# Performance work log

Measured on AMD Instinct MI355X. Metric: run time of the kernel, lower is better.

The kernel has to match this reference:

```python
import jax, jax.numpy as jnp
import numpy as np

LP = 512   # paragraph length (sequential steps)
LQ = 512   # question/context length attended over
B = 24     # batch_size global in source
IN = 150   # in_size (encoder output dim)
H = 150    # self.hidden_size = 2*75


def setup_inputs() -> dict:
    key = jax.random.key(0)
    ks = jax.random.split(key, 12)
    sc = 1.0 / np.sqrt(2 * IN)  # keep pre-activations in a sane range
    return {
        "up": jax.random.normal(ks[0], (LP, B, IN), jnp.float32),
        "uq": jax.random.normal(ks[1], (LQ, B, IN), jnp.float32),
        "v0": jax.random.normal(ks[2], (B, H), jnp.float32),
        "V": jax.random.normal(ks[3], (B, H, 1), jnp.float32),
        "Wp": jax.random.normal(ks[4], (H, 2 * IN), jnp.float32) * sc,
        "Wq": jax.random.normal(ks[5], (H, 2 * IN), jnp.float32) * sc,
        "Wv": jax.random.normal(ks[6], (H, H), jnp.float32) * sc,
        "Wg": jax.random.normal(ks[7], (4 * IN, 4 * IN), jnp.float32) * sc,
        "w_ih": jax.random.normal(ks[8], (3 * H, 2 * IN), jnp.float32) * sc,
        "w_hh": jax.random.normal(ks[9], (3 * H, H), jnp.float32) * sc,
        "b_ih": jnp.zeros((3 * H,), jnp.float32),
        "b_hh": jnp.zeros((3 * H,), jnp.float32),
    }


def _gru_cell(x, h, w_ih, w_hh, b_ih, b_hh):
    # torch.nn.GRUCell semantics
    gi = x @ w_ih.T + b_ih            # [B, 3H]
    gh = h @ w_hh.T + b_hh            # [B, 3H]
    i_r, i_z, i_n = jnp.split(gi, 3, axis=1)
    h_r, h_z, h_n = jnp.split(gh, 3, axis=1)
    r = jax.nn.sigmoid(i_r + h_r)
    z = jax.nn.sigmoid(i_z + h_z)
    n = jnp.tanh(i_n + r * h_n)
    return (1.0 - z) * n + z * h


def reference(up, uq, v0, V, Wp, Wq, Wv, Wg, w_ih, w_hh, b_ih, b_hh):
    in_size = up.shape[-1]
    # mixer = arange -> up[mixer] == up, so concat duplicates features
    Up = jnp.concatenate([up, up], axis=-1)   # [lp, B, 2*in]
    Uq = jnp.concatenate([uq, uq], axis=-1)   # [lq, B, 2*in]
    WUq = jnp.einsum('lbd,hd->lbh', Uq, Wq)   # loop-invariant Wq(Uq), [lq,B,H]
    Uq_b = Uq.transpose(1, 0, 2)              # [B, lq, 2*in]
    Vv = V[:, :, 0]                            # [B, H]

    def step(v, Up_i):                         # Up_i: [B, 2*in]
        Wup = Up_i @ Wp.T                      # [B, H]
        Wvv = v @ Wv.T                         # [B, H]
        x = jnp.tanh(WUq + Wup[None] + Wvv[None])      # [lq, B, H]
        s = jnp.einsum('lbh,bh->bl', x, Vv)            # [B, lq]
        a = jax.nn.softmax(s, axis=1)                  # [B, lq]
        c = jnp.einsum('bl,bld->bd', a, Uq_b)          # [B, 2*in]
        r = jnp.concatenate([Up_i, c], axis=1)         # [B, 4*in]
        g = jax.nn.sigmoid(r @ Wg.T)                   # [B, 4*in]
        c_ = (g * r)[:, 2 * in_size:]                  # gated attended vector
        v_new = _gru_cell(c_, v, w_ih, w_hh, b_ih, b_hh)
        return v_new, v_new

    _, vs = jax.lax.scan(step, v0, Up)  # [lp, B, H]
    # nn.Dropout in eval mode = identity
    return vs
```

## Files before the change

kernel.cpp:

```cpp
#include <hip/hip_runtime.h>
#include <hip/hip_fp16.h>

typedef _Float16 h2 __attribute__((ext_vector_type(2)));

#define OFF_EW     0u
#define OFF_UQT    983040u
#define OFF_WAV    1904640u
#define OFF_WGC    1952640u
#define OFF_WIH    1976640u
#define OFF_WQST   2048640u
#define OFF_WPC    2071140u
#define OFF_WGU    2093940u
#define OFF_UPA    2139540u
#define OFF_GU     3982740u
#define OFF_FLAG   7669140u
#define WS_FLOATS  7669156u

__device__ __forceinline__ float fast_rcp(float x) { return __builtin_amdgcn_rcpf(x); }
__device__ __forceinline__ float fast_tanh(float x) {
  return 1.f - 2.f * fast_rcp(__expf(2.f * x) + 1.f);
}
__device__ __forceinline__ float fast_sigmoid(float x) {
  return fast_rcp(1.f + __expf(-x));
}

#if defined(__has_builtin)
#if __has_builtin(__builtin_amdgcn_fdot2)
#define HAVE_FDOT2 1
#endif
#if __has_builtin(__builtin_amdgcn_s_setprio)
#define HAVE_SETPRIO 1
#endif
#endif

__device__ __forceinline__ float fdot2(h2 a, h2 b, float c) {
#ifdef HAVE_FDOT2
  return __builtin_amdgcn_fdot2(a, b, c, false);
#else
  return c + (float)a[0] * (float)b[0] + (float)a[1] * (float)b[1];
#endif
}

__global__ void prep_weights(const float* __restrict__ Wq, const float* __restrict__ Wp,
                             const float* __restrict__ Wv, const float* __restrict__ Wg,
                             const float* __restrict__ w_ih, const float* __restrict__ w_hh,
                             float* __restrict__ ws) {
  float* wqsT = ws + OFF_WQST;
  float* WPC  = ws + OFF_WPC;
  float* WGU  = ws + OFF_WGU;
  _Float16* WAV = (_Float16*)(ws + OFF_WAV);
  _Float16* WGC = (_Float16*)(ws + OFF_WGC);
  _Float16* WIHh = (_Float16*)(ws + OFF_WIH);

  int idx = blockIdx.x * blockDim.x + threadIdx.x;
  int n = gridDim.x * blockDim.x;

  for (int i = idx; i < 150 * 150; i += n) {
    int d = i / 150, h = i - d * 150;
    wqsT[i] = Wq[h * 300 + d] + Wq[h * 300 + d + 150];
  }
  for (int i = idx; i < 600 * 160; i += n) {
    int r = i / 160, h = i - r * 160;
    float v = 0.f;
    if (h < 150) v = (r < 150) ? 2.f * Wv[r * 150 + h] : w_hh[(r - 150) * 150 + h];
    WAV[i] = (_Float16)v;
  }
  for (int i = idx; i < 300 * 160; i += n) {
    int r = i / 160, h = i - r * 160;
    int row = (300 + r) * 600;
    float v = (h < 150) ? Wg[row + 300 + h] + Wg[row + 450 + h] : 0.f;
    WGC[i] = (_Float16)v;
  }
  for (int i = idx; i < 450 * 320; i += n) {
    int r = i / 320, p = i - r * 320;
    float v = (p < 300) ? w_ih[r * 300 + p] : 0.f;
    WIHh[i] = (_Float16)v;
  }
  for (int i = idx; i < 150 * 152; i += n) {
    int h = i / 152, d = i - h * 152;
    WPC[i] = (d < 150) ? 2.f * (Wp[h * 300 + d] + Wp[h * 300 + 150 + d]) : 0.f;
  }
  for (int i = idx; i < 300 * 152; i += n) {
    int r = i / 152, d = i - r * 152;
    int row = (300 + r) * 600;
    WGU[i] = (d < 150) ? Wg[row + d] + Wg[row + 150 + d] : 0.f;
  }
}

__global__ __launch_bounds__(192) void prep_ew(const float* __restrict__ uq, float* __restrict__ ws) {
  const float* wqsT = ws + OFF_WQST;
  _Float16* EW = (_Float16*)(ws + OFF_EW);
  const int l = blockIdx.x, b = blockIdx.y;
  __shared__ float sx[150], sDot[150];
  const int t = threadIdx.x;
  if (t < 150) sx[t] = uq[((size_t)l * 24 + b) * 150 + t];
  __syncthreads();
  if (t < 150) {
    float acc = 0.f;
    for (int d = 0; d < 150; ++d) acc += sx[d] * wqsT[d * 150 + t];
    sDot[t] = acc;
  }
  __syncthreads();
  if (t < 160) {
    float val = 1.f;
    if (t < 150) {
      val = __expf(2.f * sDot[t]);
      val = fminf(fmaxf(val, 1e-7f), 60000.f);
    }
    EW[((size_t)b * 512 + l) * 160 + t] = (_Float16)val;
  }
}

__global__ void prep_uqt(const float* __restrict__ uq, float* __restrict__ ws) {
  _Float16* UQT = (_Float16*)(ws + OFF_UQT);
  int idx = blockIdx.x * blockDim.x + threadIdx.x;
  int n = gridDim.x * blockDim.x;
  for (int m = idx; m < 24 * 150 * 512; m += n) {
    int b = m / (150 * 512);
    int rem = m - b * 150 * 512;
    int r = rem >> 9;
    int l = rem & 511;
    UQT[m] = (_Float16)uq[((size_t)l * 24 + b) * 150 + r];
  }
}

__global__ __launch_bounds__(256) void prep_upagu(const float* __restrict__ up, float* __restrict__ ws) {
  const int b = blockIdx.x;
  const int it = blockIdx.y;
  __shared__ float sUp[64][153];
  for (int m = threadIdx.x; m < 64 * 150; m += 256) {
    int il = m / 150, d = m - il * 150;
    sUp[il][d] = up[(((size_t)(it * 64 + il)) * 24 + b) * 150 + d];
  }
  __syncthreads();
  const float* WGU = ws + OFF_WGU;
  const float* WPC = ws + OFF_WPC;
  float* GU  = ws + OFF_GU  + ((size_t)b * 512 + it * 64) * 300;
  float* UPA = ws + OFF_UPA + ((size_t)b * 512 + it * 64) * 150;
  const int il = threadIdx.x & 63, rl = threadIdx.x >> 6;
  for (int r = rl; r < 450; r += 4) {
    const float* w = (r < 300) ? (WGU + (size_t)r * 152) : (WPC + (size_t)(r - 300) * 152);
    float acc = 0.f;
    for (int d = 0; d < 150; ++d) acc = fmaf(w[d], sUp[il][d], acc);
    if (r < 300) GU[(size_t)il * 300 + r] = acc;
    else         UPA[(size_t)il * 150 + (r - 300)] = acc;
  }
}

__global__ __launch_bounds__(1024) void pq_main(
    const float* __restrict__ v0, const float* __restrict__ Vfull,
    const float* __restrict__ b_ih, const float* __restrict__ b_hh,
    float* __restrict__ ws, float* __restrict__ out) {
  const int blk = blockIdx.x;
  const int x = blk & 7, s = blk >> 3;
  const int t3 = (s == 0) ? 0 : (s == 10) ? 1 : (s == 20) ? 2 : -1;

  if (t3 < 0) {
    if (threadIdx.x >= 64) return;
    unsigned* flag = (unsigned*)(ws + OFF_FLAG);
    const unsigned long long start = __builtin_amdgcn_s_memrealtime();
    float a0 = 0.f, a1 = 0.f, a2 = 0.f, a3 = 0.f, a4 = 0.f, a5 = 0.f, a6 = 0.f, a7 = 0.f;
    const float m = 1.0000001f, c = 0.9999999f;
    for (;;) {
      #pragma unroll 32
      for (int k = 0; k < 1024; ++k) {
        a0 = fmaf(a0, m, c); a1 = fmaf(a1, m, c); a2 = fmaf(a2, m, c); a3 = fmaf(a3, m, c);
        a4 = fmaf(a4, m, c); a5 = fmaf(a5, m, c); a6 = fmaf(a6, m, c); a7 = fmaf(a7, m, c);
      }
      if (__hip_atomic_load(flag, __ATOMIC_RELAXED, __HIP_MEMORY_SCOPE_AGENT) == 0xDEADBEEFu) break;
      if (__builtin_amdgcn_s_memrealtime() - start > 3000000ull) break;
    }
    float sink = ((a0 + a1) + (a2 + a3)) + ((a4 + a5) + (a6 + a7));
    if (sink == 123.456789f) out[0] = sink;
    return;
  }

#ifdef HAVE_SETPRIO
  __builtin_amdgcn_s_setprio(3);
#endif

  const int b = x + 8 * t3;
  const int tid = threadIdx.x;

  const _Float16* EWh  = (const _Float16*)(ws + OFF_EW);
  const _Float16* UQTh = (const _Float16*)(ws + OFF_UQT);
  const _Float16* WAV  = (const _Float16*)(ws + OFF_WAV);
  const _Float16* WIHh = (const _Float16*)(ws + OFF_WIH);

  __shared__ float sTmpA[608];
  __shared__ float eyl[160];
  __shared__ float vvl[160];
  __shared__ float sS[512];
  __shared__ float sC[152];
  __shared__ float sGip[456], sBih[456], sBhh[456];
  __shared__ float sVl[152];
  __shared__ float sRed[8], sRedB[8];
  __shared__ float sSumV;
  __shared__ h2 sAhp2[272];
  __shared__ h2 vop2[80];
  __shared__ h2 ox2[80];
  __shared__ h2 cq2[160];
  __shared__ h2 sWv2[12000];
  __shared__ h2 sWGC2[24000];
  _Float16* sAhx = (_Float16*)sAhp2;
  _Float16* vop = (_Float16*)vop2;
  _Float16* ox  = (_Float16*)ox2;
  _Float16* cq  = (_Float16*)cq2;

  const int g = tid >> 3, j = tid & 7;
  const int g16 = tid >> 4, j16 = tid & 15;

  if (tid < 160) {
    vop[tid] = (_Float16)((tid < 150) ? v0[b * 150 + tid] : 0.f);
    vvl[tid] = (tid < 150) ? Vfull[b * 150 + tid] : 0.f;
    eyl[tid] = 1.f;
  } else if (tid < 320) {
    ox[tid - 160] = (_Float16)0.f;
  } else if (tid < 640) {
    cq[tid - 320] = (_Float16)0.f;
  }
  if (tid >= 512 && tid < 968) {
    int p = tid - 512;
    sBih[p] = (p < 450) ? b_ih[p] : 0.f;
    sBhh[p] = (p < 450) ? b_hh[p] : 0.f;
  }
  if (tid < 152) sVl[tid] = (tid < 150) ? v0[b * 150 + tid] : 0.f;
  {
    const unsigned* srcv = (const unsigned*)(ws + OFF_WAV);
    unsigned* dv = (unsigned*)sWv2;
    for (int k = tid; k < 12000; k += 1024) dv[k] = srcv[k];
    const unsigned* srcg = (const unsigned*)(ws + OFF_WGC);
    unsigned* dg = (unsigned*)sWGC2;
    for (int k = tid; k < 24000; k += 1024) dg[k] = srcg[k];
  }
  __syncthreads();
  if (tid >= 192 && tid < 256) {
    int ln = tid - 192;
    float sm = 0.f;
    for (int h = ln; h < 150; h += 64) sm += vvl[h];
    #pragma unroll
    for (int off = 32; off; off >>= 1) sm += __shfl_xor(sm, off, 64);
    if (ln == 0) sSumV = sm;
  }
  __syncthreads();

  for (int i = 0; i < 512; ++i) {
    {
      float ua0 = 0.f, ua1 = 0.f;
      if (j == 0) {
        const float* UPA = ws + OFF_UPA + ((size_t)b * 512 + i) * 150;
        ua0 = UPA[g];
        if (g < 22) ua1 = UPA[128 + g];
      }
      h2 va[10];
      #pragma unroll
      for (int t = 0; t < 10; ++t) va[t] = vop2[j * 10 + t];
      #pragma unroll
      for (int it = 0; it < 5; ++it) {
        const int r = g + (it << 7);
        if (r < 600) {
          h2 w[10];
          if (r < 150) {
            const h2* wp = sWv2 + r * 80 + j * 10;
            #pragma unroll
            for (int t = 0; t < 10; ++t) w[t] = wp[t];
          } else {
            const h2* wp = (const h2*)WAV + (size_t)r * 80 + j * 10;
            #pragma unroll
            for (int t = 0; t < 10; ++t) w[t] = wp[t];
          }
          float acc = 0.f;
          #pragma unroll
          for (int t = 0; t < 10; ++t) acc = fdot2(w[t], va[t], acc);
          acc += __shfl_xor(acc, 1, 64);
          acc += __shfl_xor(acc, 2, 64);
          acc += __shfl_xor(acc, 4, 64);
          if (j == 0) {
            if (r >= 150) sTmpA[r] = acc;
            else eyl[r] = fminf(__expf(((it == 0) ? ua0 : ua1) + acc), 1e30f);
          }
        }
      }
    }
    __syncthreads();
    {
      float ey[20], vv[20];
      #pragma unroll
      for (int t = 0; t < 20; ++t) { ey[t] = eyl[j * 20 + t]; vv[t] = vvl[j * 20 + t]; }
      #pragma unroll
      for (int it = 0; it < 4; ++it) {
        const int r = g + (it << 7);
        const h2* wp = (const h2*)(EWh + ((size_t)b * 512 + r) * 160) + j * 10;
        h2 w[10];
        #pragma unroll
        for (int t = 0; t < 10; ++t) w[t] = wp[t];
        float acc = 0.f;
        #pragma unroll
        for (int t = 0; t < 10; ++t) {
          float x1 = fmaf((float)w[t][0], ey[2 * t],     1.f);
          float y1 = fmaf((float)w[t][1], ey[2 * t + 1], 1.f);
          float num = fmaf(vv[2 * t], y1, vv[2 * t + 1] * x1);
          acc = fmaf(num, fast_rcp(x1 * y1), acc);
        }
        acc += __shfl_xor(acc, 1, 64);
        acc += __shfl_xor(acc, 2, 64);
        acc += __shfl_xor(acc, 4, 64);
        if (j == 0) sS[r] = sSumV - 2.f * acc;
      }
    }
    __syncthreads();
    {
      const bool act = tid < 512;
      float sv = act ? sS[tid] : -3.4e38f;
      float m = sv;
      #pragma unroll
      for (int off = 32; off; off >>= 1) m = fmaxf(m, __shfl_xor(m, off, 64));
      float e = act ? __expf(sv - m) : 0.f;
      float z = e;
      #pragma unroll
      for (int off = 32; off; off >>= 1) z += __shfl_xor(z, off, 64);
      if (act && (tid & 63) == 0) { sRed[tid >> 6] = m; sRedB[tid >> 6] = z; }
      __syncthreads();
      if (act) {
        float M = sRed[0];
        #pragma unroll
        for (int w = 1; w < 8; ++w) M = fmaxf(M, sRed[w]);
        float Z = 0.f;
        #pragma unroll
        for (int w = 0; w < 8; ++w) Z += sRedB[w] * __expf(sRed[w] - M);
        float a = (e * __expf(m - M)) * fast_rcp(Z);
        sAhx[(tid >> 5) * 34 + (tid & 31)] = (_Float16)a;
      }
    }
    __syncthreads();
    {
      h2 aa[16];
      #pragma unroll
      for (int t = 0; t < 16; ++t) aa[t] = sAhp2[j16 * 17 + t];
      #pragma unroll
      for (int it = 0; it < 3; ++it) {
        const int r = g16 + (it << 6);
        if (r < 150) {
          const h2* wp = (const h2*)(UQTh + ((size_t)b * 150 + r) * 512) + j16 * 16;
          h2 w[16];
          #pragma unroll
          for (int t = 0; t < 16; ++t) w[t] = wp[t];
          float acc = 0.f;
          #pragma unroll
          for (int t = 0; t < 16; ++t) acc = fdot2(aa[t], w[t], acc);
          acc += __shfl_xor(acc, 1, 64);
          acc += __shfl_xor(acc, 2, 64);
          acc += __shfl_xor(acc, 4, 64);
          acc += __shfl_xor(acc, 8, 64);
          if (j16 == 0) {
            sC[r] = acc;
            ox[r] = (_Float16)acc;
          }
        }
      }
    }
    __syncthreads();
    {
      float gu0 = 0.f, gu1 = 0.f, gu2 = 0.f;
      if (j == 0) {
        const float* GUp = ws + OFF_GU + ((size_t)b * 512 + i) * 300;
        gu0 = GUp[g];
        gu1 = GUp[128 + g];
        if (g < 44) gu2 = GUp[256 + g];
      }
      h2 xa[10];
      #pragma unroll
      for (int t = 0; t < 10; ++t) xa[t] = ox2[j * 10 + t];
      #pragma unroll
      for (int it = 0; it < 3; ++it) {
        const int r = g + (it << 7);
        if (r < 300) {
          const h2* wp = sWGC2 + r * 80 + j * 10;
          h2 w[10];
          #pragma unroll
          for (int t = 0; t < 10; ++t) w[t] = wp[t];
          float acc = 0.f;
          #pragma unroll
          for (int t = 0; t < 10; ++t) acc = fdot2(w[t], xa[t], acc);
          acc += __shfl_xor(acc, 1, 64);
          acc += __shfl_xor(acc, 2, 64);
          acc += __shfl_xor(acc, 4, 64);
          if (j == 0) {
            float gg = fast_sigmoid(acc + ((it == 0) ? gu0 : (it == 1) ? gu1 : gu2));
            int cj = (r >= 150) ? r - 150 : r;
            cq[r] = (_Float16)(gg * sC[cj]);
          }
        }
      }
    }
    __syncthreads();
    {
      h2 xa[20];
      #pragma unroll
      for (int t = 0; t < 20; ++t) xa[t] = cq2[j * 20 + t];
      #pragma unroll
      for (int it = 0; it < 4; ++it) {
        const int r = g + (it << 7);
        if (r < 450) {
          const h2* wp = (const h2*)WIHh + (size_t)r * 160 + j * 20;
          h2 w[20];
          #pragma unroll
          for (int t = 0; t < 20; ++t) w[t] = wp[t];
          float acc = 0.f;
          #pragma unroll
          for (int t = 0; t < 20; ++t) acc = fdot2(w[t], xa[t], acc);
          acc += __shfl_xor(acc, 1, 64);
          acc += __shfl_xor(acc, 2, 64);
          acc += __shfl_xor(acc, 4, 64);
          if (j == 0) sGip[r] = acc;
        }
      }
    }
    __syncthreads();
    if (tid < 150) {
      const int h = tid;
      float gh_r = sTmpA[150 + h] + sBhh[h];
      float gh_z = sTmpA[300 + h] + sBhh[150 + h];
      float gh_n = sTmpA[450 + h] + sBhh[300 + h];
      float rg = fast_sigmoid(sGip[h]       + sBih[h]       + gh_r);
      float zg = fast_sigmoid(sGip[150 + h] + sBih[150 + h] + gh_z);
      float nn = fast_tanh(sGip[300 + h] + sBih[300 + h] + rg * gh_n);
      float vn = (1.f - zg) * nn + zg * sVl[h];
      sVl[h] = vn;
      vop[h] = (_Float16)vn;
      out[((size_t)i * 24 + b) * 150 + h] = vn;
    }
    __syncthreads();
  }

  if (b == 0 && tid == 0) {
    __hip_atomic_store((unsigned*)(ws + OFF_FLAG), 0xDEADBEEFu,
                       __ATOMIC_RELAXED, __HIP_MEMORY_SCOPE_AGENT);
  }
}

extern "C" void kernel_launch(void* const* d_in, const int* in_sizes, int n_in,
                              void* d_out, int out_size, void* d_ws, size_t ws_size,
                              hipStream_t stream) {
  const float* up   = (const float*)d_in[0];
  const float* uq   = (const float*)d_in[1];
  const float* v0   = (const float*)d_in[2];
  const float* V    = (const float*)d_in[3];
  const float* Wp   = (const float*)d_in[4];
  const float* Wq   = (const float*)d_in[5];
  const float* Wv   = (const float*)d_in[6];
  const float* Wg   = (const float*)d_in[7];
  const float* w_ih = (const float*)d_in[8];
  const float* w_hh = (const float*)d_in[9];
  const float* b_ih = (const float*)d_in[10];
  const float* b_hh = (const float*)d_in[11];
  float* ws  = (float*)d_ws;
  float* out = (float*)d_out;

  if (ws_size < (size_t)WS_FLOATS * sizeof(float)) return;

  prep_weights<<<256, 256, 0, stream>>>(Wq, Wp, Wv, Wg, w_ih, w_hh, ws);
  prep_uqt<<<512, 256, 0, stream>>>(uq, ws);
  prep_ew<<<dim3(512, 24), 192, 0, stream>>>(uq, ws);
  prep_upagu<<<dim3(24, 8), 256, 0, stream>>>(up, ws);
  pq_main<<<256, 1024, 0, stream>>>(v0, V, b_ih, b_hh, ws, out);
}
```

Baseline: 6.792 ms.

## Pre-tile global weight and Uq layouts for coalesced wide vector loads in recurrent loop

Prep kernels now write the w_hh, w_ih, EW and Uq^T arrays in a lane-interleaved tiled layout. In that layout each lane of a wave reads consecutive 8- or 4-half vectors, so the per-step global loads in the sequential loop coalesce into wide transactions instead of strided per-lane row reads. The GRU biases are folded into the weight matrices as an extra column multiplied by a constant-1 input element, which removes the separate bias loads and adds. Row-to-thread mappings change to match: 4 lanes per row for the v projections and 16 rows per wave. The cost is extra padded workspace and more complex prep indexing.

```diff
diff --git a/kernel.cpp b/kernel.cpp
--- a/kernel.cpp
+++ b/kernel.cpp
@@ -2,19 +2,22 @@
 #include <hip/hip_fp16.h>
 
 typedef _Float16 h2 __attribute__((ext_vector_type(2)));
-
-#define OFF_EW     0u
-#define OFF_UQT    983040u
-#define OFF_WAV    1904640u
-#define OFF_WGC    1952640u
-#define OFF_WIH    1976640u
-#define OFF_WQST   2048640u
-#define OFF_WPC    2071140u
-#define OFF_WGU    2093940u
-#define OFF_UPA    2139540u
-#define OFF_GU     3982740u
-#define OFF_FLAG   7669140u
-#define WS_FLOATS  7669156u
+typedef _Float16 h4 __attribute__((ext_vector_type(4)));
+typedef _Float16 h8 __attribute__((ext_vector_type(8)));
+
+#define OFF_EWT    0u
+#define OFF_UQTT   983040u
+#define OFF_WHHT   2162688u
+#define OFF_WIHT   2203648u
+#define OFF_WV2    2285568u
+#define OFF_WGC    2298768u
+#define OFF_WQST   2322768u
+#define OFF_WPC    2345268u
+#define OFF_WGU    2368068u
+#define OFF_UPA    2413668u
+#define OFF_GU     4256868u
+#define OFF_FLAG   7943268u
+#define WS_FLOATS  7943284u
 
 __device__ __forceinline__ float fast_rcp(float x) { return __builtin_amdgcn_rcpf(x); }
 __device__ __forceinline__ float fast_tanh(float x) {
@@ -44,13 +47,15 @@
 __global__ void prep_weights(const float* __restrict__ Wq, const float* __restrict__ Wp,
                              const float* __restrict__ Wv, const float* __restrict__ Wg,
                              const float* __restrict__ w_ih, const float* __restrict__ w_hh,
+                             const float* __restrict__ b_ih, const float* __restrict__ b_hh,
                              float* __restrict__ ws) {
   float* wqsT = ws + OFF_WQST;
   float* WPC  = ws + OFF_WPC;
   float* WGU  = ws + OFF_WGU;
-  _Float16* WAV = (_Float16*)(ws + OFF_WAV);
-  _Float16* WGC = (_Float16*)(ws + OFF_WGC);
-  _Float16* WIHh = (_Float16*)(ws + OFF_WIH);
+  _Float16* WV2  = (_Float16*)(ws + OFF_WV2);
+  _Float16* WGC  = (_Float16*)(ws + OFF_WGC);
+  _Float16* WHHT = (_Float16*)(ws + OFF_WHHT);
+  _Float16* WIHT = (_Float16*)(ws + OFF_WIHT);
 
   int idx = blockIdx.x * blockDim.x + threadIdx.x;
   int n = gridDim.x * blockDim.x;
@@ -59,11 +64,21 @@
     int d = i / 150, h = i - d * 150;
     wqsT[i] = Wq[h * 300 + d] + Wq[h * 300 + d + 150];
   }
-  for (int i = idx; i < 600 * 160; i += n) {
-    int r = i / 160, h = i - r * 160;
+  for (int i = idx; i < 150 * 176; i += n) {
+    int r = i / 176, h = i - r * 176;
+    WV2[i] = (_Float16)((h < 150) ? 2.f * Wv[r * 150 + h] : 0.f);
+  }
+  for (int i = idx; i < 512 * 160; i += n) {
+    int r512 = i / 160, h = i - r512 * 160;
     float v = 0.f;
-    if (h < 150) v = (r < 150) ? 2.f * Wv[r * 150 + h] : w_hh[(r - 150) * 150 + h];
-    WAV[i] = (_Float16)v;
+    if (r512 < 450) {
+      if (h < 150) v = w_hh[r512 * 150 + h];
+      else if (h == 150) v = b_hh[r512];
+    }
+    int it = r512 >> 8, rr = r512 & 255, wv = rr >> 4, lr4 = rr & 15;
+    int j4 = h / 40, hh = h % 40, k = hh >> 3, c = hh & 7;
+    int lane = lr4 * 4 + j4;
+    WHHT[(size_t)(it * 16 + wv) * 2560 + k * 512 + lane * 8 + c] = (_Float16)v;
   }
   for (int i = idx; i < 300 * 160; i += n) {
     int r = i / 160, h = i - r * 160;
@@ -71,10 +86,17 @@
     float v = (h < 150) ? Wg[row + 300 + h] + Wg[row + 450 + h] : 0.f;
     WGC[i] = (_Float16)v;
   }
-  for (int i = idx; i < 450 * 320; i += n) {
-    int r = i / 320, p = i - r * 320;
-    float v = (p < 300) ? w_ih[r * 300 + p] : 0.f;
-    WIHh[i] = (_Float16)v;
+  for (int i = idx; i < 512 * 320; i += n) {
+    int r512 = i / 320, h = i - r512 * 320;
+    float v = 0.f;
+    if (r512 < 450) {
+      if (h < 300) v = w_ih[r512 * 300 + h];
+      else if (h == 300) v = b_ih[r512];
+    }
+    int it = r512 >> 7, rr = r512 & 127, wv = rr >> 3, lr = rr & 7;
+    int j = h / 40, hh = h % 40, k = hh >> 3, c = hh & 7;
+    int lane = lr * 8 + j;
+    WIHT[(size_t)(it * 16 + wv) * 2560 + k * 512 + lane * 8 + c] = (_Float16)v;
   }
   for (int i = idx; i < 150 * 152; i += n) {
     int h = i / 152, d = i - h * 152;
@@ -89,7 +111,7 @@
 
 __global__ __launch_bounds__(192) void prep_ew(const float* __restrict__ uq, float* __restrict__ ws) {
   const float* wqsT = ws + OFF_WQST;
-  _Float16* EW = (_Float16*)(ws + OFF_EW);
+  _Float16* EWT = (_Float16*)(ws + OFF_EWT);
   const int l = blockIdx.x, b = blockIdx.y;
   __shared__ float sx[150], sDot[150];
   const int t = threadIdx.x;
@@ -107,20 +129,27 @@
       val = __expf(2.f * sDot[t]);
       val = fminf(fmaxf(val, 1e-7f), 60000.f);
     }
-    EW[((size_t)b * 512 + l) * 160 + t] = (_Float16)val;
+    int j = t / 20, tt = t % 20, k = tt >> 2, c = tt & 3;
+    int lane = (l & 7) * 8 + j;
+    EWT[((size_t)b * 64 + (l >> 7) * 16 + ((l >> 3) & 15)) * 1280 + k * 256 + lane * 4 + c] =
+        (_Float16)val;
   }
 }
 
 __global__ void prep_uqt(const float* __restrict__ uq, float* __restrict__ ws) {
-  _Float16* UQT = (_Float16*)(ws + OFF_UQT);
+  _Float16* UQTT = (_Float16*)(ws + OFF_UQTT);
   int idx = blockIdx.x * blockDim.x + threadIdx.x;
   int n = gridDim.x * blockDim.x;
-  for (int m = idx; m < 24 * 150 * 512; m += n) {
-    int b = m / (150 * 512);
-    int rem = m - b * 150 * 512;
+  for (int m = idx; m < 24 * 192 * 512; m += n) {
+    int b = m / (192 * 512);
+    int rem = m - b * 192 * 512;
     int r = rem >> 9;
-    int l = rem & 511;
-    UQT[m] = (_Float16)uq[((size_t)l * 24 + b) * 150 + r];
+    int q = rem & 511;
+    float v = (r < 150) ? uq[((size_t)q * 24 + b) * 150 + r] : 0.f;
+    int it = r >> 6, rr = r & 63, wv = rr >> 2, lr = rr & 3;
+    int j16 = q >> 5, k = (q & 31) >> 3, c = q & 7;
+    int lane = lr * 16 + j16;
+    UQTT[((size_t)b * 48 + it * 16 + wv) * 2048 + k * 512 + lane * 8 + c] = (_Float16)v;
   }
 }
 
@@ -149,7 +178,6 @@
 
 __global__ __launch_bounds__(1024) void pq_main(
     const float* __restrict__ v0, const float* __restrict__ Vfull,
-    const float* __restrict__ b_ih, const float* __restrict__ b_hh,
     float* __restrict__ ws, float* __restrict__ out) {
   const int blk = blockIdx.x;
   const int x = blk & 7, s = blk >> 3;
@@ -182,55 +210,55 @@
   const int b = x + 8 * t3;
   const int tid = threadIdx.x;
 
-  const _Float16* EWh  = (const _Float16*)(ws + OFF_EW);
-  const _Float16* UQTh = (const _Float16*)(ws + OFF_UQT);
-  const _Float16* WAV  = (const _Float16*)(ws + OFF_WAV);
-  const _Float16* WIHh = (const _Float16*)(ws + OFF_WIH);
-
+  const h4* EWT4  = (const h4*)(ws + OFF_EWT);
+  const h8* UQTT8 = (const h8*)(ws + OFF_UQTT);
+  const h8* WHHT8 = (const h8*)(ws + OFF_WHHT);
+  const h8* WIHT8 = (const h8*)(ws + OFF_WIHT);
+  const float* UPAb = ws + OFF_UPA + (size_t)b * 512 * 150;
+  const float* GUb  = ws + OFF_GU  + (size_t)b * 512 * 300;
+
+  __shared__ h8 sWv8[3300];
+  __shared__ h4 sWGC4[12000];
   __shared__ float sTmpA[608];
   __shared__ float eyl[160];
   __shared__ float vvl[160];
   __shared__ float sS[512];
   __shared__ float sC[152];
-  __shared__ float sGip[456], sBih[456], sBhh[456];
+  __shared__ float sGip[456];
   __shared__ float sVl[152];
   __shared__ float sRed[8], sRedB[8];
   __shared__ float sSumV;
-  __shared__ h2 sAhp2[272];
-  __shared__ h2 vop2[80];
-  __shared__ h2 ox2[80];
-  __shared__ h2 cq2[160];
-  __shared__ h2 sWv2[12000];
-  __shared__ h2 sWGC2[24000];
-  _Float16* sAhx = (_Float16*)sAhp2;
-  _Float16* vop = (_Float16*)vop2;
-  _Float16* ox  = (_Float16*)ox2;
-  _Float16* cq  = (_Float16*)cq2;
-
+  __shared__ h4 sAh4[144];
+  __shared__ h8 vop8[20];
+  __shared__ h8 cq8[40];
+  __shared__ h4 ox4[40];
+  _Float16* sAhx = (_Float16*)sAh4;
+  _Float16* vop  = (_Float16*)vop8;
+  _Float16* cqh  = (_Float16*)cq8;
+  _Float16* oxh  = (_Float16*)ox4;
+
+  const int l  = tid & 63, wv = tid >> 6;
   const int g = tid >> 3, j = tid & 7;
+  const int g4 = tid >> 2, j4 = tid & 3;
   const int g16 = tid >> 4, j16 = tid & 15;
 
   if (tid < 160) {
-    vop[tid] = (_Float16)((tid < 150) ? v0[b * 150 + tid] : 0.f);
+    vop[tid] = (_Float16)((tid < 150) ? v0[b * 150 + tid] : (tid == 150 ? 1.f : 0.f));
     vvl[tid] = (tid < 150) ? Vfull[b * 150 + tid] : 0.f;
     eyl[tid] = 1.f;
   } else if (tid < 320) {
-    ox[tid - 160] = (_Float16)0.f;
+    oxh[tid - 160] = (_Float16)0.f;
   } else if (tid < 640) {
-    cq[tid - 320] = (_Float16)0.f;
-  }
-  if (tid >= 512 && tid < 968) {
-    int p = tid - 512;
-    sBih[p] = (p < 450) ? b_ih[p] : 0.f;
-    sBhh[p] = (p < 450) ? b_hh[p] : 0.f;
+    int p = tid - 320;
+    cqh[p] = (_Float16)((p == 300) ? 1.f : 0.f);
   }
   if (tid < 152) sVl[tid] = (tid < 150) ? v0[b * 150 + tid] : 0.f;
   {
-    const unsigned* srcv = (const unsigned*)(ws + OFF_WAV);
-    unsigned* dv = (unsigned*)sWv2;
-    for (int k = tid; k < 12000; k += 1024) dv[k] = srcv[k];
+    const unsigned* srcv = (const unsigned*)(ws + OFF_WV2);
+    unsigned* dv = (unsigned*)sWv8;
+    for (int k = tid; k < 13200; k += 1024) dv[k] = srcv[k];
     const unsigned* srcg = (const unsigned*)(ws + OFF_WGC);
-    unsigned* dg = (unsigned*)sWGC2;
+    unsigned* dg = (unsigned*)sWGC4;
     for (int k = tid; k < 24000; k += 1024) dg[k] = srcg[k];
   }
   __syncthreads();
@@ -246,66 +274,66 @@
 
   for (int i = 0; i < 512; ++i) {
     {
-      float ua0 = 0.f, ua1 = 0.f;
-      if (j == 0) {
-        const float* UPA = ws + OFF_UPA + ((size_t)b * 512 + i) * 150;
-        ua0 = UPA[g];
-        if (g < 22) ua1 = UPA[128 + g];
-      }
-      h2 va[10];
-      #pragma unroll
-      for (int t = 0; t < 10; ++t) va[t] = vop2[j * 10 + t];
-      #pragma unroll
-      for (int it = 0; it < 5; ++it) {
-        const int r = g + (it << 7);
-        if (r < 600) {
-          h2 w[10];
-          if (r < 150) {
-            const h2* wp = sWv2 + r * 80 + j * 10;
-            #pragma unroll
-            for (int t = 0; t < 10; ++t) w[t] = wp[t];
-          } else {
-            const h2* wp = (const h2*)WAV + (size_t)r * 80 + j * 10;
-            #pragma unroll
-            for (int t = 0; t < 10; ++t) w[t] = wp[t];
-          }
+      h8 va8[5];
+      #pragma unroll
+      for (int k = 0; k < 5; ++k) va8[k] = vop8[j4 * 5 + k];
+      const h2* va = (const h2*)va8;
+      float ua = 0.f;
+      if (j4 == 0 && g4 < 150) ua = UPAb[(size_t)i * 150 + g4];
+      if (g4 < 150) {
+        h8 w8[5];
+        #pragma unroll
+        for (int k = 0; k < 5; ++k) w8[k] = sWv8[g4 * 22 + j4 * 5 + k];
+        const h2* wh = (const h2*)w8;
+        float acc = 0.f;
+        #pragma unroll
+        for (int t = 0; t < 20; ++t) acc = fdot2(wh[t], va[t], acc);
+        acc += __shfl_xor(acc, 1, 64);
+        acc += __shfl_xor(acc, 2, 64);
+        if (j4 == 0) eyl[g4] = fminf(__expf(ua + acc), 1e30f);
+      }
+      #pragma unroll
+      for (int it = 0; it < 2; ++it) {
+        if (it == 0 || wv < 13) {
+          const h8* tp = WHHT8 + (size_t)(it * 16 + wv) * 320 + l;
+          h8 w8[5];
+          #pragma unroll
+          for (int k = 0; k < 5; ++k) w8[k] = tp[k * 64];
+          const h2* wh = (const h2*)w8;
           float acc = 0.f;
           #pragma unroll
-          for (int t = 0; t < 10; ++t) acc = fdot2(w[t], va[t], acc);
+          for (int t = 0; t < 20; ++t) acc = fdot2(wh[t], va[t], acc);
           acc += __shfl_xor(acc, 1, 64);
           acc += __shfl_xor(acc, 2, 64);
-          acc += __shfl_xor(acc, 4, 64);
-          if (j == 0) {
-            if (r >= 150) sTmpA[r] = acc;
-            else eyl[r] = fminf(__expf(((it == 0) ? ua0 : ua1) + acc), 1e30f);
-          }
+          const int r = 150 + it * 256 + g4;
+          if (j4 == 0 && r < 600) sTmpA[r] = acc;
         }
       }
     }
     __syncthreads();
     {
-      float ey[20], vv[20];
-      #pragma unroll
-      for (int t = 0; t < 20; ++t) { ey[t] = eyl[j * 20 + t]; vv[t] = vvl[j * 20 + t]; }
+      float ey[20], vvr[20];
+      #pragma unroll
+      for (int t = 0; t < 20; ++t) { ey[t] = eyl[j * 20 + t]; vvr[t] = vvl[j * 20 + t]; }
+      const h4* ewt = EWT4 + ((size_t)b * 64 + wv) * 320 + l;
       #pragma unroll
       for (int it = 0; it < 4; ++it) {
-        const int r = g + (it << 7);
-        const h2* wp = (const h2*)(EWh + ((size_t)b * 512 + r) * 160) + j * 10;
-        h2 w[10];
+        h4 w4[5];
         #pragma unroll
-        for (int t = 0; t < 10; ++t) w[t] = wp[t];
+        for (int k = 0; k < 5; ++k) w4[k] = ewt[it * 5120 + k * 64];
+        const h2* wh = (const h2*)w4;
         float acc = 0.f;
         #pragma unroll
         for (int t = 0; t < 10; ++t) {
-          float x1 = fmaf((float)w[t][0], ey[2 * t],     1.f);
-          float y1 = fmaf((float)w[t][1], ey[2 * t + 1], 1.f);
-          float num = fmaf(vv[2 * t], y1, vv[2 * t + 1] * x1);
+          float x1 = fmaf((float)wh[t][0], ey[2 * t],     1.f);
+          float y1 = fmaf((float)wh[t][1], ey[2 * t + 1], 1.f);
+          float num = fmaf(vvr[2 * t], y1, vvr[2 * t + 1] * x1);
           acc = fmaf(num, fast_rcp(x1 * y1), acc);
         }
         acc += __shfl_xor(acc, 1, 64);
         acc += __shfl_xor(acc, 2, 64);
         acc += __shfl_xor(acc, 4, 64);
-        if (j == 0) sS[r] = sSumV - 2.f * acc;
+        if (j == 0) sS[it * 128 + g] = sSumV - 2.f * acc;
       }
     }
     __syncthreads();
@@ -329,32 +357,34 @@
         #pragma unroll
         for (int w = 0; w < 8; ++w) Z += sRedB[w] * __expf(sRed[w] - M);
         float a = (e * __expf(m - M)) * fast_rcp(Z);
-        sAhx[(tid >> 5) * 34 + (tid & 31)] = (_Float16)a;
+        sAhx[(tid >> 5) * 36 + (tid & 31)] = (_Float16)a;
       }
     }
     __syncthreads();
     {
-      h2 aa[16];
-      #pragma unroll
-      for (int t = 0; t < 16; ++t) aa[t] = sAhp2[j16 * 17 + t];
+      h4 aa4[8];
+      #pragma unroll
+      for (int t = 0; t < 8; ++t) aa4[t] = sAh4[j16 * 9 + t];
+      const h2* aa = (const h2*)aa4;
+      const h8* uqt = UQTT8 + ((size_t)b * 48 + wv) * 256 + l;
       #pragma unroll
       for (int it = 0; it < 3; ++it) {
-        const int r = g16 + (it << 6);
-        if (r < 150) {
-          const h2* wp = (const h2*)(UQTh + ((size_t)b * 150 + r) * 512) + j16 * 16;
-          h2 w[16];
-          #pragma unroll
-          for (int t = 0; t < 16; ++t) w[t] = wp[t];
+        if (it < 2 || wv < 6) {
+          h8 w8[4];
+          #pragma unroll
+          for (int k = 0; k < 4; ++k) w8[k] = uqt[it * 4096 + k * 64];
+          const h2* wh = (const h2*)w8;
           float acc = 0.f;
           #pragma unroll
-          for (int t = 0; t < 16; ++t) acc = fdot2(aa[t], w[t], acc);
+          for (int t = 0; t < 16; ++t) acc = fdot2(aa[t], wh[t], acc);
           acc += __shfl_xor(acc, 1, 64);
           acc += __shfl_xor(acc, 2, 64);
           acc += __shfl_xor(acc, 4, 64);
           acc += __shfl_xor(acc, 8, 64);
-          if (j16 == 0) {
+          const int r = it * 64 + g16;
+          if (j16 == 0 && r < 150) {
             sC[r] = acc;
-            ox[r] = (_Float16)acc;
+            oxh[r] = (_Float16)acc;
           }
         }
       }
@@ -363,68 +393,71 @@
     {
       float gu0 = 0.f, gu1 = 0.f, gu2 = 0.f;
       if (j == 0) {
-        const float* GUp = ws + OFF_GU + ((size_t)b * 512 + i) * 300;
+        const float* GUp = GUb + (size_t)i * 300;
         gu0 = GUp[g];
         gu1 = GUp[128 + g];
         if (g < 44) gu2 = GUp[256 + g];
       }
-      h2 xa[10];
-      #pragma unroll
-      for (int t = 0; t < 10; ++t) xa[t] = ox2[j * 10 + t];
+      h4 xa4[5];
+      #pragma unroll
+      for (int t = 0; t < 5; ++t) xa4[t] = ox4[j * 5 + t];
+      const h2* xa = (const h2*)xa4;
       #pragma unroll
       for (int it = 0; it < 3; ++it) {
         const int r = g + (it << 7);
         if (r < 300) {
-          const h2* wp = sWGC2 + r * 80 + j * 10;
-          h2 w[10];
-          #pragma unroll
-          for (int t = 0; t < 10; ++t) w[t] = wp[t];
+          h4 w4[5];
+          #pragma unroll
+          for (int k = 0; k < 5; ++k) w4[k] = sWGC4[r * 40 + j * 5 + k];
+          const h2* wh = (const h2*)w4;
           float acc = 0.f;
           #pragma unroll
-          for (int t = 0; t < 10; ++t) acc = fdot2(w[t], xa[t], acc);
+          for (int t = 0; t < 10; ++t) acc = fdot2(wh[t], xa[t], acc);
           acc += __shfl_xor(acc, 1, 64);
           acc += __shfl_xor(acc, 2, 64);
           acc += __shfl_xor(acc, 4, 64);
           if (j == 0) {
             float gg = fast_sigmoid(acc + ((it == 0) ? gu0 : (it == 1) ? gu1 : gu2));
             int cj = (r >= 150) ? r - 150 : r;
-            cq[r] = (_Float16)(gg * sC[cj]);
+            cqh[r] = (_Float16)(gg * sC[cj]);
           }
         }
       }
     }
     __syncthreads();
     {
-      h2 xa[20];
-      #pragma unroll
-      for (int t = 0; t < 20; ++t) xa[t] = cq2[j * 20 + t];
+      h8 xq8[5];
+      #pragma unroll
+      for (int k = 0; k < 5; ++k) xq8[k] = cq8[j * 5 + k];
+      const h2* xa = (const h2*)xq8;
+      const h8* wih = WIHT8 + wv * 320 + l;
       #pragma unroll
       for (int it = 0; it < 4; ++it) {
-        const int r = g + (it << 7);
-        if (r < 450) {
-          const h2* wp = (const h2*)WIHh + (size_t)r * 160 + j * 20;
-          h2 w[20];
-          #pragma unroll
-          for (int t = 0; t < 20; ++t) w[t] = wp[t];
+        if (it < 3 || wv < 9) {
+          h8 w8[5];
+          #pragma unroll
+          for (int k = 0; k < 5; ++k) w8[k] = wih[(size_t)it * 5120 + k * 64];
+          const h2* wh = (const h2*)w8;
           float acc = 0.f;
           #pragma unroll
-          for (int t = 0; t < 20; ++t) acc = fdot2(w[t], xa[t], acc);
+          for (int t = 0; t < 20; ++t) acc = fdot2(wh[t], xa[t], acc);
           acc += __shfl_xor(acc, 1, 64);
           acc += __shfl_xor(acc, 2, 64);
           acc += __shfl_xor(acc, 4, 64);
-          if (j == 0) sGip[r] = acc;
+          const int r = it * 128 + g;
+          if (j == 0 && r < 450) sGip[r] = acc;
         }
       }
     }
     __syncthreads();
     if (tid < 150) {
       const int h = tid;
-      float gh_r = sTmpA[150 + h] + sBhh[h];
-      float gh_z = sTmpA[300 + h] + sBhh[150 + h];
-      float gh_n = sTmpA[450 + h] + sBhh[300 + h];
-      float rg = fast_sigmoid(sGip[h]       + sBih[h]       + gh_r);
-      float zg = fast_sigmoid(sGip[150 + h] + sBih[150 + h] + gh_z);
-      float nn = fast_tanh(sGip[300 + h] + sBih[300 + h] + rg * gh_n);
+      float gh_r = sTmpA[150 + h];
+      float gh_z = sTmpA[300 + h];
+      float gh_n = sTmpA[450 + h];
+      float rg = fast_sigmoid(sGip[h] + gh_r);
+      float zg = fast_sigmoid(sGip[150 + h] + gh_z);
+      float nn = fast_tanh(sGip[300 + h] + rg * gh_n);
       float vn = (1.f - zg) * nn + zg * sVl[h];
       sVl[h] = vn;
       vop[h] = (_Float16)vn;
@@ -459,9 +492,9 @@
 
   if (ws_size < (size_t)WS_FLOATS * sizeof(float)) return;
 
-  prep_weights<<<256, 256, 0, stream>>>(Wq, Wp, Wv, Wg, w_ih, w_hh, ws);
+  prep_weights<<<256, 256, 0, stream>>>(Wq, Wp, Wv, Wg, w_ih, w_hh, b_ih, b_hh, ws);
   prep_uqt<<<512, 256, 0, stream>>>(uq, ws);
   prep_ew<<<dim3(512, 24), 192, 0, stream>>>(uq, ws);
   prep_upagu<<<dim3(24, 8), 256, 0, stream>>>(up, ws);
-  pq_main<<<256, 1024, 0, stream>>>(v0, V, b_ih, b_hh, ws, out);
-}
+  pq_main<<<256, 1024, 0, stream>>>(v0, V, ws, out);
+}
```

After: 8.305 ms. 22.3% more time.

## Software-prefetch next-phase weights and inputs into registers before each barrier

Applied to the files above, without the earlier changes.

Each phase of the sequential step loop now issues the global loads for the following phase (EW rows, UqT rows, W_ih rows, next-step Wav rows and Up/gate-precompute slices) into register arrays before the current phase's barrier and compute. The aim is to hide global/L2 load latency behind the preceding phase instead of stalling at the start of each phase. In exchange, register pressure rises considerably (about 130 extra h2 values per thread), which could cause spills or lower occupancy in a 1024-thread block.

```diff
diff --git a/kernel.cpp b/kernel.cpp
--- a/kernel.cpp
+++ b/kernel.cpp
@@ -186,6 +186,8 @@
   const _Float16* UQTh = (const _Float16*)(ws + OFF_UQT);
   const _Float16* WAV  = (const _Float16*)(ws + OFF_WAV);
   const _Float16* WIHh = (const _Float16*)(ws + OFF_WIH);
+  const float* UPAb = ws + OFF_UPA + (size_t)b * 512 * 150;
+  const float* GUb  = ws + OFF_GU  + (size_t)b * 512 * 300;
 
   __shared__ float sTmpA[608];
   __shared__ float eyl[160];
@@ -244,13 +246,37 @@
   }
   __syncthreads();
 
+  h2 wavR[4][10];
+  float uaR0 = 0.f, uaR1 = 0.f;
+  h2 ewR[4][10];
+  h2 uqR[3][16];
+  h2 wihR[4][20];
+  float guR0 = 0.f, guR1 = 0.f, guR2 = 0.f;
+
+  {
+    #pragma unroll
+    for (int it = 1; it < 5; ++it) {
+      const int r = g + (it << 7);
+      if (r >= 150 && r < 600) {
+        const h2* wp = (const h2*)WAV + (size_t)r * 80 + j * 10;
+        #pragma unroll
+        for (int t = 0; t < 10; ++t) wavR[it - 1][t] = wp[t];
+      }
+    }
+    if (j == 0) {
+      uaR0 = UPAb[g];
+      if (g < 22) uaR1 = UPAb[128 + g];
+    }
+  }
+
   for (int i = 0; i < 512; ++i) {
     {
-      float ua0 = 0.f, ua1 = 0.f;
-      if (j == 0) {
-        const float* UPA = ws + OFF_UPA + ((size_t)b * 512 + i) * 150;
-        ua0 = UPA[g];
-        if (g < 22) ua1 = UPA[128 + g];
+      #pragma unroll
+      for (int it = 0; it < 4; ++it) {
+        const int r = g + (it << 7);
+        const h2* wp = (const h2*)(EWh + ((size_t)b * 512 + r) * 160) + j * 10;
+        #pragma unroll
+        for (int t = 0; t < 10; ++t) ewR[it][t] = wp[t];
       }
       h2 va[10];
       #pragma unroll
@@ -265,9 +291,8 @@
             #pragma unroll
             for (int t = 0; t < 10; ++t) w[t] = wp[t];
           } else {
-            const h2* wp = (const h2*)WAV + (size_t)r * 80 + j * 10;
             #pragma unroll
-            for (int t = 0; t < 10; ++t) w[t] = wp[t];
+            for (int t = 0; t < 10; ++t) w[t] = wavR[it - 1][t];
           }
           float acc = 0.f;
           #pragma unroll
@@ -277,28 +302,33 @@
           acc += __shfl_xor(acc, 4, 64);
           if (j == 0) {
             if (r >= 150) sTmpA[r] = acc;
-            else eyl[r] = fminf(__expf(((it == 0) ? ua0 : ua1) + acc), 1e30f);
+            else eyl[r] = fminf(__expf(((it == 0) ? uaR0 : uaR1) + acc), 1e30f);
           }
         }
       }
     }
     __syncthreads();
     {
+      #pragma unroll
+      for (int it = 0; it < 3; ++it) {
+        const int r = g16 + (it << 6);
+        if (r < 150) {
+          const h2* wp = (const h2*)(UQTh + ((size_t)b * 150 + r) * 512) + j16 * 16;
+          #pragma unroll
+          for (int t = 0; t < 16; ++t) uqR[it][t] = wp[t];
+        }
+      }
       float ey[20], vv[20];
       #pragma unroll
       for (int t = 0; t < 20; ++t) { ey[t] = eyl[j * 20 + t]; vv[t] = vvl[j * 20 + t]; }
       #pragma unroll
       for (int it = 0; it < 4; ++it) {
         const int r = g + (it << 7);
-        const h2* wp = (const h2*)(EWh + ((size_t)b * 512 + r) * 160) + j * 10;
-        h2 w[10];
-        #pragma unroll
-        for (int t = 0; t < 10; ++t) w[t] = wp[t];
         float acc = 0.f;
         #pragma unroll
         for (int t = 0; t < 10; ++t) {
-          float x1 = fmaf((float)w[t][0], ey[2 * t],     1.f);
-          float y1 = fmaf((float)w[t][1], ey[2 * t + 1], 1.f);
+          float x1 = fmaf((float)ewR[it][t][0], ey[2 * t],     1.f);
+          float y1 = fmaf((float)ewR[it][t][1], ey[2 * t + 1], 1.f);
           float num = fmaf(vv[2 * t], y1, vv[2 * t + 1] * x1);
           acc = fmaf(num, fast_rcp(x1 * y1), acc);
         }
@@ -310,6 +340,12 @@
     }
     __syncthreads();
     {
+      if (j == 0) {
+        const float* GUp = GUb + (size_t)i * 300;
+        guR0 = GUp[g];
+        guR1 = GUp[128 + g];
+        if (g < 44) guR2 = GUp[256 + g];
+      }
       const bool act = tid < 512;
       float sv = act ? sS[tid] : -3.4e38f;
       float m = sv;
@@ -341,13 +377,9 @@
       for (int it = 0; it < 3; ++it) {
         const int r = g16 + (it << 6);
         if (r < 150) {
-          const h2* wp = (const h2*)(UQTh + ((size_t)b * 150 + r) * 512) + j16 * 16;
-          h2 w[16];
-          #pragma unroll
-          for (int t = 0; t < 16; ++t) w[t] = wp[t];
           float acc = 0.f;
           #pragma unroll
-          for (int t = 0; t < 16; ++t) acc = fdot2(aa[t], w[t], acc);
+          for (int t = 0; t < 16; ++t) acc = fdot2(aa[t], uqR[it][t], acc);
           acc += __shfl_xor(acc, 1, 64);
           acc += __shfl_xor(acc, 2, 64);
           acc += __shfl_xor(acc, 4, 64);
@@ -361,12 +393,14 @@
     }
     __syncthreads();
     {
-      float gu0 = 0.f, gu1 = 0.f, gu2 = 0.f;
-      if (j == 0) {
-        const float* GUp = ws + OFF_GU + ((size_t)b * 512 + i) * 300;
-        gu0 = GUp[g];
-        gu1 = GUp[128 + g];
-        if (g < 44) gu2 = GUp[256 + g];
+      #pragma unroll
+      for (int it = 0; it < 4; ++it) {
+        const int r = g + (it << 7);
+        if (r < 450) {
+          const h2* wp = (const h2*)WIHh + (size_t)r * 160 + j * 20;
+          #pragma unroll
+          for (int t = 0; t < 20; ++t) wihR[it][t] = wp[t];
+        }
       }
       h2 xa[10];
       #pragma unroll
@@ -386,7 +420,7 @@
           acc += __shfl_xor(acc, 2, 64);
           acc += __shfl_xor(acc, 4, 64);
           if (j == 0) {
-            float gg = fast_sigmoid(acc + ((it == 0) ? gu0 : (it == 1) ? gu1 : gu2));
+            float gg = fast_sigmoid(acc + ((it == 0) ? guR0 : (it == 1) ? guR1 : guR2));
             int cj = (r >= 150) ? r - 150 : r;
             cq[r] = (_Float16)(gg * sC[cj]);
           }
@@ -395,6 +429,20 @@
     }
     __syncthreads();
     {
+      const int inx = (i + 1 < 512) ? i + 1 : i;
+      #pragma unroll
+      for (int it = 1; it < 5; ++it) {
+        const int r = g + (it << 7);
+        if (r >= 150 && r < 600) {
+          const h2* wp = (const h2*)WAV + (size_t)r * 80 + j * 10;
+          #pragma unroll
+          for (int t = 0; t < 10; ++t) wavR[it - 1][t] = wp[t];
+        }
+      }
+      if (j == 0) {
+        uaR0 = UPAb[(size_t)inx * 150 + g];
+        if (g < 22) uaR1 = UPAb[(size_t)inx * 150 + 128 + g];
+      }
       h2 xa[20];
       #pragma unroll
       for (int t = 0; t < 20; ++t) xa[t] = cq2[j * 20 + t];
@@ -402,13 +450,9 @@
       for (int it = 0; it < 4; ++it) {
         const int r = g + (it << 7);
         if (r < 450) {
-          const h2* wp = (const h2*)WIHh + (size_t)r * 160 + j * 20;
-          h2 w[20];
-          #pragma unroll
-          for (int t = 0; t < 20; ++t) w[t] = wp[t];
           float acc = 0.f;
           #pragma unroll
-          for (int t = 0; t < 20; ++t) acc = fdot2(w[t], xa[t], acc);
+          for (int t = 0; t < 20; ++t) acc = fdot2(wihR[it][t], xa[t], acc);
           acc += __shfl_xor(acc, 1, 64);
           acc += __shfl_xor(acc, 2, 64);
           acc += __shfl_xor(acc, 4, 64);
```

Result: slower. 14.49 ms (+113.3%).

## Split each batch's recurrence across two workgroups with global-memory flag handshakes

Applied to the files above, without the earlier changes.

Each batch element's sequential GRU/attention step is now shared between two workgroups: each computes half of the hidden rows, half of the attention scores, half of the context and gate outputs. They exchange partial results through a global workspace buffer and synchronise five times per step with release/acquire flag spinning. The aim is to halve the per-step matvec work on the critical path. In exchange it adds five cross-CU handshakes per step through L2/global memory, whose latency can exceed the compute saved.

```diff
diff --git a/kernel.cpp b/kernel.cpp
--- a/kernel.cpp
+++ b/kernel.cpp
@@ -14,7 +14,9 @@
 #define OFF_UPA    2139540u
 #define OFF_GU     3982740u
 #define OFF_FLAG   7669140u
-#define WS_FLOATS  7669156u
+#define OFF_EXG    7669156u
+#define OFF_XFLG   7706020u
+#define WS_FLOATS  7706432u
 
 __device__ __forceinline__ float fast_rcp(float x) { return __builtin_amdgcn_rcpf(x); }
 __device__ __forceinline__ float fast_tanh(float x) {
@@ -84,6 +86,14 @@
     int r = i / 152, d = i - r * 152;
     int row = (300 + r) * 600;
     WGU[i] = (d < 150) ? Wg[row + d] + Wg[row + 150 + d] : 0.f;
+  }
+  {
+    unsigned* xf = (unsigned*)(ws + OFF_XFLG);
+    for (int i = idx; i < 24 * 16; i += n) xf[i] = 0u;
+  }
+  for (int i = idx; i < 24 * 10; i += n) {
+    int bb = i / 10, t = i - bb * 10;
+    ws[OFF_EXG + (size_t)bb * 1536 + 150 + t] = 1.0f;
   }
 }
 
@@ -153,7 +163,10 @@
     float* __restrict__ ws, float* __restrict__ out) {
   const int blk = blockIdx.x;
   const int x = blk & 7, s = blk >> 3;
-  const int t3 = (s == 0) ? 0 : (s == 10) ? 1 : (s == 20) ? 2 : -1;
+  int t3 = -1;
+  if (s == 0 || s == 1) t3 = 0;
+  else if (s == 10 || s == 11) t3 = 1;
+  else if (s == 20 || s == 21) t3 = 2;
 
   if (t3 < 0) {
     if (threadIdx.x >= 64) return;
@@ -179,20 +192,38 @@
   __builtin_amdgcn_s_setprio(3);
 #endif
 
+  const int hf = s & 1;
   const int b = x + 8 * t3;
   const int tid = threadIdx.x;
+
+  const int EYB = hf ? 80 : 0, EYW = hf ? 70 : 80;
+  const int PEYB = hf ? 0 : 80, PEYW = hf ? 80 : 70;
+  const int CQB = hf ? 160 : 0, CQW = hf ? 140 : 160;
+  const int NA  = 4 * EYW;
+  const int NP4 = 3 * EYW;
 
   const _Float16* EWh  = (const _Float16*)(ws + OFF_EW);
   const _Float16* UQTh = (const _Float16*)(ws + OFF_UQT);
   const _Float16* WAV  = (const _Float16*)(ws + OFF_WAV);
   const _Float16* WIHh = (const _Float16*)(ws + OFF_WIH);
+  const float* UPAb = ws + OFF_UPA + (size_t)b * 512 * 150;
+  const float* GUb  = ws + OFF_GU  + (size_t)b * 512 * 300;
+
+  float* EX = ws + OFF_EXG + (size_t)b * 1536;
+  float* exEY = EX;
+  float* exS  = EX + 160;
+  float* exC  = EX + 672;
+  float* exCQ = EX + 824;
+  float* exV  = EX + 1128;
+  unsigned* FLG = (unsigned*)(ws + OFF_XFLG);
+  unsigned* myflag = FLG + (b * 16 + hf * 8);
+  unsigned* pflag  = FLG + (b * 16 + (1 - hf) * 8);
 
   __shared__ float sTmpA[608];
-  __shared__ float eyl[160];
   __shared__ float vvl[160];
-  __shared__ float sS[512];
   __shared__ float sC[152];
-  __shared__ float sGip[456], sBih[456], sBhh[456];
+  __shared__ float sGip[456];
+  __shared__ float sBih[456], sBhh[456];
   __shared__ float sVl[152];
   __shared__ float sRed[8], sRedB[8];
   __shared__ float sSumV;
@@ -213,7 +244,6 @@
   if (tid < 160) {
     vop[tid] = (_Float16)((tid < 150) ? v0[b * 150 + tid] : 0.f);
     vvl[tid] = (tid < 150) ? Vfull[b * 150 + tid] : 0.f;
-    eyl[tid] = 1.f;
   } else if (tid < 320) {
     ox[tid - 160] = (_Float16)0.f;
   } else if (tid < 640) {
@@ -244,53 +274,73 @@
   }
   __syncthreads();
 
+  #define XSYNC(K)                                                                   \
+    __syncthreads();                                                                 \
+    if (tid == 0) {                                                                  \
+      __threadfence();                                                               \
+      __hip_atomic_store(myflag + (K), (unsigned)(i + 1), __ATOMIC_RELEASE,          \
+                         __HIP_MEMORY_SCOPE_AGENT);                                  \
+      const unsigned long long t0 = __builtin_amdgcn_s_memrealtime();                \
+      while (__hip_atomic_load(pflag + (K), __ATOMIC_ACQUIRE,                        \
+                               __HIP_MEMORY_SCOPE_AGENT) < (unsigned)(i + 1)) {      \
+        __builtin_amdgcn_s_sleep(1);                                                 \
+        if (__builtin_amdgcn_s_memrealtime() - t0 > 20000000ull) break;     \
+      }                                                                              \
+    }                                                                                \
+    __syncthreads();
+
   for (int i = 0; i < 512; ++i) {
     {
-      float ua0 = 0.f, ua1 = 0.f;
-      if (j == 0) {
-        const float* UPA = ws + OFF_UPA + ((size_t)b * 512 + i) * 150;
-        ua0 = UPA[g];
-        if (g < 22) ua1 = UPA[128 + g];
-      }
       h2 va[10];
       #pragma unroll
       for (int t = 0; t < 10; ++t) va[t] = vop2[j * 10 + t];
       #pragma unroll
-      for (int it = 0; it < 5; ++it) {
-        const int r = g + (it << 7);
-        if (r < 600) {
-          h2 w[10];
-          if (r < 150) {
-            const h2* wp = sWv2 + r * 80 + j * 10;
+      for (int it = 0; it < 3; ++it) {
+        const int idx = g + (it << 7);
+        if (idx < NA) {
+          const int k = (idx >= 3 * EYW) ? 3 : (idx >= 2 * EYW) ? 2 : (idx >= EYW) ? 1 : 0;
+          const int o = idx - k * EYW;
+          float acc = 0.f;
+          if (k == 0) {
+            const int row = EYB + o;
+            const h2* wp = sWv2 + row * 80 + j * 10;
+            h2 w[10];
             #pragma unroll
             for (int t = 0; t < 10; ++t) w[t] = wp[t];
+            #pragma unroll
+            for (int t = 0; t < 10; ++t) acc = fdot2(w[t], va[t], acc);
+            acc += __shfl_xor(acc, 1, 64);
+            acc += __shfl_xor(acc, 2, 64);
+            acc += __shfl_xor(acc, 4, 64);
+            if (j == 0) {
+              float ua = UPAb[(size_t)i * 150 + row];
+              exEY[row] = fminf(__expf(ua + acc), 1e30f);
+            }
           } else {
-            const h2* wp = (const h2*)WAV + (size_t)r * 80 + j * 10;
+            const int rt = k * 150 + EYB + o;
+            const h2* wp = (const h2*)WAV + (size_t)rt * 80 + j * 10;
+            h2 w[10];
             #pragma unroll
             for (int t = 0; t < 10; ++t) w[t] = wp[t];
-          }
-          float acc = 0.f;
-          #pragma unroll
-          for (int t = 0; t < 10; ++t) acc = fdot2(w[t], va[t], acc);
-          acc += __shfl_xor(acc, 1, 64);
-          acc += __shfl_xor(acc, 2, 64);
-          acc += __shfl_xor(acc, 4, 64);
-          if (j == 0) {
-            if (r >= 150) sTmpA[r] = acc;
-            else eyl[r] = fminf(__expf(((it == 0) ? ua0 : ua1) + acc), 1e30f);
+            #pragma unroll
+            for (int t = 0; t < 10; ++t) acc = fdot2(w[t], va[t], acc);
+            acc += __shfl_xor(acc, 1, 64);
+            acc += __shfl_xor(acc, 2, 64);
+            acc += __shfl_xor(acc, 4, 64);
+            if (j == 0) sTmpA[rt] = acc;
           }
         }
       }
     }
-    __syncthreads();
+    XSYNC(0)
     {
       float ey[20], vv[20];
       #pragma unroll
-      for (int t = 0; t < 20; ++t) { ey[t] = eyl[j * 20 + t]; vv[t] = vvl[j * 20 + t]; }
-      #pragma unroll
-      for (int it = 0; it < 4; ++it) {
-        const int r = g + (it << 7);
-        const h2* wp = (const h2*)(EWh + ((size_t)b * 512 + r) * 160) + j * 10;
+      for (int t = 0; t < 20; ++t) { ey[t] = exEY[j * 20 + t]; vv[t] = vvl[j * 20 + t]; }
+      #pragma unroll
+      for (int it = 0; it < 2; ++it) {
+        const int l = 256 * hf + g + (it << 7);
+        const h2* wp = (const h2*)(EWh + ((size_t)b * 512 + l) * 160) + j * 10;
         h2 w[10];
         #pragma unroll
         for (int t = 0; t < 10; ++t) w[t] = wp[t];
@@ -305,13 +355,13 @@
         acc += __shfl_xor(acc, 1, 64);
         acc += __shfl_xor(acc, 2, 64);
         acc += __shfl_xor(acc, 4, 64);
-        if (j == 0) sS[r] = sSumV - 2.f * acc;
-      }
-    }
-    __syncthreads();
+        if (j == 0) exS[l] = sSumV - 2.f * acc;
+      }
+    }
+    XSYNC(1)
     {
       const bool act = tid < 512;
-      float sv = act ? sS[tid] : -3.4e38f;
+      float sv = act ? exS[tid] : -3.4e38f;
       float m = sv;
       #pragma unroll
       for (int off = 32; off; off >>= 1) m = fmaxf(m, __shfl_xor(m, off, 64));
@@ -338,9 +388,10 @@
       #pragma unroll
       for (int t = 0; t < 16; ++t) aa[t] = sAhp2[j16 * 17 + t];
       #pragma unroll
-      for (int it = 0; it < 3; ++it) {
-        const int r = g16 + (it << 6);
-        if (r < 150) {
+      for (int it = 0; it < 2; ++it) {
+        const int idx = g16 + (it << 6);
+        if (idx < EYW) {
+          const int r = EYB + idx;
           const h2* wp = (const h2*)(UQTh + ((size_t)b * 150 + r) * 512) + j16 * 16;
           h2 w[16];
           #pragma unroll
@@ -352,29 +403,26 @@
           acc += __shfl_xor(acc, 2, 64);
           acc += __shfl_xor(acc, 4, 64);
           acc += __shfl_xor(acc, 8, 64);
-          if (j16 == 0) {
-            sC[r] = acc;
-            ox[r] = (_Float16)acc;
-          }
+          if (j16 == 0) exC[r] = acc;
         }
       }
+    }
+    XSYNC(2)
+    if (tid < 152) {
+      float f = (tid < 150) ? exC[tid] : 0.f;
+      sC[tid] = f;
+      ox[tid] = (_Float16)f;
     }
     __syncthreads();
     {
-      float gu0 = 0.f, gu1 = 0.f, gu2 = 0.f;
-      if (j == 0) {
-        const float* GUp = ws + OFF_GU + ((size_t)b * 512 + i) * 300;
-        gu0 = GUp[g];
-        gu1 = GUp[128 + g];
-        if (g < 44) gu2 = GUp[256 + g];
-      }
       h2 xa[10];
       #pragma unroll
       for (int t = 0; t < 10; ++t) xa[t] = ox2[j * 10 + t];
       #pragma unroll
-      for (int it = 0; it < 3; ++it) {
-        const int r = g + (it << 7);
-        if (r < 300) {
+      for (int it = 0; it < 2; ++it) {
+        const int idx = g + (it << 7);
+        if (idx < CQW) {
+          const int r = CQB + idx;
           const h2* wp = sWGC2 + r * 80 + j * 10;
           h2 w[10];
           #pragma unroll
@@ -386,22 +434,28 @@
           acc += __shfl_xor(acc, 2, 64);
           acc += __shfl_xor(acc, 4, 64);
           if (j == 0) {
-            float gg = fast_sigmoid(acc + ((it == 0) ? gu0 : (it == 1) ? gu1 : gu2));
+            float gu = GUb[(size_t)i * 300 + r];
+            float gg = fast_sigmoid(acc + gu);
             int cj = (r >= 150) ? r - 150 : r;
-            cq[r] = (_Float16)(gg * sC[cj]);
+            exCQ[r] = gg * sC[cj];
           }
         }
       }
     }
+    XSYNC(3)
+    if (tid < 300) cq[tid] = (_Float16)exCQ[tid];
     __syncthreads();
     {
       h2 xa[20];
       #pragma unroll
       for (int t = 0; t < 20; ++t) xa[t] = cq2[j * 20 + t];
       #pragma unroll
-      for (int it = 0; it < 4; ++it) {
-        const int r = g + (it << 7);
-        if (r < 450) {
+      for (int it = 0; it < 2; ++it) {
+        const int idx = g + (it << 7);
+        if (idx < NP4) {
+          const int k = (idx >= 2 * EYW) ? 2 : (idx >= EYW) ? 1 : 0;
+          const int o = idx - k * EYW;
+          const int r = k * 150 + EYB + o;
           const h2* wp = (const h2*)WIHh + (size_t)r * 160 + j * 20;
           h2 w[20];
           #pragma unroll
@@ -417,8 +471,8 @@
       }
     }
     __syncthreads();
-    if (tid < 150) {
-      const int h = tid;
+    if (tid < EYW) {
+      const int h = EYB + tid;
       float gh_r = sTmpA[150 + h] + sBhh[h];
       float gh_z = sTmpA[300 + h] + sBhh[150 + h];
       float gh_n = sTmpA[450 + h] + sBhh[300 + h];
@@ -428,15 +482,22 @@
       float vn = (1.f - zg) * nn + zg * sVl[h];
       sVl[h] = vn;
       vop[h] = (_Float16)vn;
+      exV[h] = vn;
       out[((size_t)i * 24 + b) * 150 + h] = vn;
     }
+    XSYNC(4)
+    if (tid < PEYW) {
+      const int hp = PEYB + tid;
+      vop[hp] = (_Float16)exV[hp];
+    }
     __syncthreads();
   }
 
-  if (b == 0 && tid == 0) {
+  if (b == 0 && hf == 0 && tid == 0) {
     __hip_atomic_store((unsigned*)(ws + OFF_FLAG), 0xDEADBEEFu,
                        __ATOMIC_RELAXED, __HIP_MEMORY_SCOPE_AGENT);
   }
+  #undef XSYNC
 }
 
 extern "C" void kernel_launch(void* const* d_in, const int* in_sizes, int n_in,
```

After: 9.850 ms. 1.45x slower.
